# Optimization experiments

Measured on AMD Instinct MI355X. Metric: run time of the kernel, lower is better.

Reference implementation:

```python
import jax, jax.numpy as jnp
import numpy as np

COMMITMENT_COST = 0.25
NUM_EMBEDDINGS = 8192
EMBEDDING_DIM = 256


def setup_inputs() -> dict:
    key = jax.random.key(0)
    kx, ke = jax.random.split(key)
    x = jax.random.normal(kx, (16, 1024, EMBEDDING_DIM), dtype=jnp.float32)
    # nn.Embedding weight initialized uniform(-1/K, 1/K)
    embedding = jax.random.uniform(
        ke, (NUM_EMBEDDINGS, EMBEDDING_DIM), dtype=jnp.float32,
        minval=-1.0 / NUM_EMBEDDINGS, maxval=1.0 / NUM_EMBEDDINGS)
    return {"x": x, "embedding": embedding}


def reference(x, embedding):
    x_shape = x.shape
    D = embedding.shape[1]
    K = embedding.shape[0]
    flat_x = x.reshape(-1, D)                      # [N, D]
    N = flat_x.shape[0]

    distances = (jnp.sum(flat_x ** 2, axis=1, keepdims=True)
                 + jnp.sum(embedding ** 2, axis=1)
                 - 2.0 * jnp.matmul(flat_x, embedding.T))
    encoding_indices = jnp.argmin(distances, axis=1)  # [N]

    # one-hot @ embedding == gather
    quantized = embedding[encoding_indices].reshape(x_shape)

    sg = jax.lax.stop_gradient
    e_latent_loss = jnp.mean((sg(quantized) - x) ** 2)
    q_latent_loss = jnp.mean((quantized - sg(x)) ** 2)
    loss = q_latent_loss + COMMITMENT_COST * e_latent_loss

    # straight-through estimator
    quantized_st = x + sg(quantized - x)

    # perplexity from mean one-hot usage
    counts = jnp.zeros((K,), dtype=jnp.float32).at[encoding_indices].add(1.0)
    avg_probs = counts / N
    perplexity = jnp.exp(-jnp.sum(avg_probs * jnp.log(avg_probs + 1e-10)))

    return quantized_st.reshape(x_shape), loss, perplexity
```

## Files before the change

kernel.cpp:

```cpp
#include <hip/hip_runtime.h>


#define VQ_N 16384
#define VQ_D 256
#define VQ_K 8192

typedef __attribute__((ext_vector_type(4))) int i32x4;

#define SX 22.0f
#define SEF 1040384.0f
#define ENSCALE 11444224.0

__device__ inline int q8(float f, float scale) {
  return __float2int_rn(fminf(fmaxf(f * scale, -127.f), 127.f));
}

__device__ inline void gl_lds16(const void* g, void* l) {
  __builtin_amdgcn_global_load_lds(
      (const __attribute__((address_space(1))) unsigned int*)g,
      (__attribute__((address_space(3))) unsigned int*)l, 16, 0, 0);
}
__device__ inline void gl_lds4(const void* g, void* l) {
  __builtin_amdgcn_global_load_lds(
      (const __attribute__((address_space(1))) unsigned int*)g,
      (__attribute__((address_space(3))) unsigned int*)l, 4, 0, 0);
}

__global__ __launch_bounds__(256) void vq_pack(
    const float* __restrict__ E, signed char* __restrict__ Ebs,
    int* __restrict__ en_int, double* __restrict__ loss_sum,
    int* __restrict__ hist, unsigned int* __restrict__ ticket) {
  const int gid = blockIdx.x * 256 + threadIdx.x;
  if (gid < VQ_K) hist[gid] = 0;
  if (gid == 0) { *loss_sum = 0.0; *ticket = 0u; }
  const int code = gid >> 4;
  const int chunk = gid & 15;
  const float* src = E + (size_t)code * VQ_D + chunk * 16;
  double s = 0.0;
  unsigned int w[4];
#pragma unroll
  for (int v = 0; v < 4; ++v) {
    const float4 f = *(const float4*)(src + v * 4);
    s += (double)f.x * f.x + (double)f.y * f.y + (double)f.z * f.z +
         (double)f.w * f.w;
    const int q0 = q8(f.x, SEF), q1 = q8(f.y, SEF);
    const int q2 = q8(f.z, SEF), q3 = q8(f.w, SEF);
    w[v] = (unsigned)(q0 & 255) | ((unsigned)(q1 & 255) << 8) |
           ((unsigned)(q2 & 255) << 16) | ((unsigned)(q3 & 255) << 24);
  }
  const size_t off =
      ((size_t)(code >> 4) * 16 + chunk) * 256 + (size_t)(code & 15) * 16;
  *(uint4*)(Ebs + off) = make_uint4(w[0], w[1], w[2], w[3]);
#pragma unroll
  for (int m = 1; m <= 8; m <<= 1) s += __shfl_xor(s, m, 64);
  if (chunk == 0) en_int[code] = (int)__double2int_rn(s * ENSCALE);
}

__global__ __launch_bounds__(256, 2) void vq_score(
    const float* __restrict__ X, const signed char* __restrict__ Ebs,
    const int* __restrict__ en_int, unsigned long long* __restrict__ best64) {
  __shared__ __align__(16) signed char bbuf[2][16384];
  __shared__ __align__(16) int enl[1024];

  const int tid = threadIdx.x;
  const int wave = tid >> 6;
  const int lane = tid & 63;
  const int quad = lane >> 4;
  const int c15 = lane & 15;
  const int rowblk = blockIdx.x >> 3;
  const int q = blockIdx.x & 7;
  const int r0 = rowblk * 256;
  const int qcode = q * 1024;
  const signed char* ebase = Ebs + (size_t)qcode * 256;

  {
    const int* ens = en_int + qcode + wave * 64 + lane;
#pragma unroll
    for (int j = 0; j < 4; ++j)
      gl_lds4(ens + j * 256, enl + j * 256 + wave * 64);
    const signed char* bs = ebase + wave * 1024 + lane * 16;
#pragma unroll
    for (int j = 0; j < 4; ++j)
      gl_lds16(bs + j * 4096, &bbuf[0][j * 4096 + wave * 1024]);
  }

  i32x4 af[4][4];
#pragma unroll
  for (int t = 0; t < 4; ++t) {
    const float* xr =
        X + (size_t)(r0 + wave * 64 + t * 16 + c15) * VQ_D + quad * 16;
#pragma unroll
    for (int m = 0; m < 4; ++m) {
      const float* p = xr + m * 64;
      i32x4 pk;
#pragma unroll
      for (int v = 0; v < 4; ++v) {
        const float4 f = *(const float4*)(p + v * 4);
        pk[v] = (q8(f.x, SX) & 255) | ((q8(f.y, SX) & 255) << 8) |
                ((q8(f.z, SX) & 255) << 16) | ((q8(f.w, SX) & 255) << 24);
      }
      af[t][m] = pk;
    }
  }

  int best_s[4][4];
  int best_i[4][4];
#pragma unroll
  for (int t = 0; t < 4; ++t)
#pragma unroll
    for (int r = 0; r < 4; ++r) { best_s[t][r] = 0x7fffffff; best_i[t][r] = 0; }

#pragma unroll 1
  for (int c = 0; c < 16; ++c) {
    __syncthreads();
    if (c + 1 < 16) {
      const signed char* bs =
          ebase + (c + 1) * 16384 + wave * 1024 + lane * 16;
#pragma unroll
      for (int j = 0; j < 4; ++j)
        gl_lds16(bs + j * 4096, &bbuf[(c + 1) & 1][j * 4096 + wave * 1024]);
    }
    const signed char* cb = &bbuf[c & 1][0];
#pragma unroll
    for (int g = 0; g < 4; ++g) {
      i32x4 bfr[4];
#pragma unroll
      for (int m = 0; m < 4; ++m)
        bfr[m] = *(const i32x4*)(cb + g * 4096 + m * 1024 + lane * 16);
      const int en = enl[(c * 4 + g) * 16 + c15];
      i32x4 a0 = {0, 0, 0, 0}, a1 = {0, 0, 0, 0};
      i32x4 a2 = {0, 0, 0, 0}, a3 = {0, 0, 0, 0};
#pragma unroll
      for (int m = 0; m < 4; ++m) {
        a0 = __builtin_amdgcn_mfma_i32_16x16x64_i8(af[0][m], bfr[m], a0, 0, 0, 0);
        a1 = __builtin_amdgcn_mfma_i32_16x16x64_i8(af[1][m], bfr[m], a1, 0, 0, 0);
        a2 = __builtin_amdgcn_mfma_i32_16x16x64_i8(af[2][m], bfr[m], a2, 0, 0, 0);
        a3 = __builtin_amdgcn_mfma_i32_16x16x64_i8(af[3][m], bfr[m], a3, 0, 0, 0);
      }
      const int code = qcode + (c * 4 + g) * 16 + c15;
#pragma unroll
      for (int r = 0; r < 4; ++r) {
        int s;
        s = en - a0[r];
        if (s < best_s[0][r]) { best_s[0][r] = s; best_i[0][r] = code; }
        s = en - a1[r];
        if (s < best_s[1][r]) { best_s[1][r] = s; best_i[1][r] = code; }
        s = en - a2[r];
        if (s < best_s[2][r]) { best_s[2][r] = s; best_i[2][r] = code; }
        s = en - a3[r];
        if (s < best_s[3][r]) { best_s[3][r] = s; best_i[3][r] = code; }
      }
    }
  }

#pragma unroll
  for (int t = 0; t < 4; ++t)
#pragma unroll
    for (int r = 0; r < 4; ++r) {
      int s = best_s[t][r];
      int i = best_i[t][r];
#pragma unroll
      for (int m = 1; m <= 8; m <<= 1) {
        const int os = __shfl_xor(s, m, 64);
        const int oi = __shfl_xor(i, m, 64);
        if (os < s || (os == s && oi < i)) { s = os; i = oi; }
      }
      if (c15 == 0) {
        const int row = r0 + wave * 64 + t * 16 + quad * 4 + r;
        best64[(size_t)q * VQ_N + row] =
            ((unsigned long long)((unsigned)s ^ 0x80000000u) << 32) |
            (unsigned)i;
      }
    }
}

__global__ __launch_bounds__(256) void vq_gather_fin(
    const float* __restrict__ X, const float* __restrict__ E,
    const unsigned long long* __restrict__ best64, float* __restrict__ outq,
    double* __restrict__ loss_sum, int* __restrict__ hist,
    unsigned int* __restrict__ ticket, float* __restrict__ out) {
  __shared__ double wsum[4];
  __shared__ double part[256];
  __shared__ int sdone;
  const int wid = threadIdx.x >> 6;
  const int lane = threadIdx.x & 63;
  const int gw = blockIdx.x * 4 + wid;
  double acc = 0.0;
#pragma unroll 4
  for (int row = gw; row < VQ_N; row += 2048) {
    unsigned long long v =
        (lane < 8) ? best64[(size_t)lane * VQ_N + row] : ~0ULL;
#pragma unroll
    for (int m = 1; m <= 4; m <<= 1) {
      const unsigned long long ov = __shfl_xor(v, m, 64);
      if (ov < v) v = ov;
    }
    v = __shfl(v, 0, 64);
    const int k = (int)(v & 0xFFFFFFFFu);
    if (lane == 0)
      __hip_atomic_fetch_add(&hist[k], 1, __ATOMIC_RELAXED,
                             __HIP_MEMORY_SCOPE_AGENT);
    const float4 qv = *(const float4*)(E + (size_t)k * VQ_D + lane * 4);
    const float4 xv = *(const float4*)(X + (size_t)row * VQ_D + lane * 4);
    *(float4*)(outq + (size_t)row * VQ_D + lane * 4) = qv;
    const double dx = (double)qv.x - xv.x, dy = (double)qv.y - xv.y;
    const double dz = (double)qv.z - xv.z, dw = (double)qv.w - xv.w;
    acc += dx * dx + dy * dy + dz * dz + dw * dw;
  }
#pragma unroll
  for (int off = 32; off > 0; off >>= 1) acc += __shfl_down(acc, off, 64);
  if (lane == 0) wsum[wid] = acc;
  __syncthreads();
  if (threadIdx.x == 0) {
    atomicAdd(loss_sum, wsum[0] + wsum[1] + wsum[2] + wsum[3]);
    __threadfence();
    const unsigned int old = __hip_atomic_fetch_add(
        ticket, 1u, __ATOMIC_ACQ_REL, __HIP_MEMORY_SCOPE_AGENT);
    sdone = (old == 511u) ? 1 : 0;
  }
  __syncthreads();

  if (sdone) {
    const int tx = threadIdx.x;
    double s = 0.0;
    for (int k = tx; k < VQ_K; k += 256) {
      const int c = __hip_atomic_load(&hist[k], __ATOMIC_RELAXED,
                                      __HIP_MEMORY_SCOPE_AGENT);
      if (c > 0) {
        const double pr = (double)c * (1.0 / (double)VQ_N);
        s += pr * log(pr + 1e-10);
      }
    }
    part[tx] = s;
    __syncthreads();
    for (int off = 128; off > 0; off >>= 1) {
      if (tx < off) part[tx] += part[tx + off];
      __syncthreads();
    }
    if (tx == 0) {
      const double ls = __hip_atomic_load(loss_sum, __ATOMIC_RELAXED,
                                          __HIP_MEMORY_SCOPE_AGENT);
      out[(size_t)VQ_N * VQ_D] =
          (float)(1.25 * ls / ((double)VQ_N * (double)VQ_D));
      out[(size_t)VQ_N * VQ_D + 1] = (float)exp(-part[0]);
    }
  }
}

extern "C" void kernel_launch(void* const* d_in, const int* in_sizes, int n_in,
                              void* d_out, int out_size, void* d_ws,
                              size_t ws_size, hipStream_t stream) {
  const float* X = (const float*)d_in[0];
  const float* E = (const float*)d_in[1];
  float* out = (float*)d_out;

  char* ws = (char*)d_ws;
  signed char* Ebs = (signed char*)ws;
  int* en_int = (int*)(ws + 2097152);
  double* loss_sum = (double*)(ws + 2129920);
  int* hist = (int*)(ws + 2129984);
  unsigned int* ticket = (unsigned int*)(ws + 2162752);
  unsigned long long* best64 =
      (unsigned long long*)(ws + 2162816);

  vq_pack<<<512, 256, 0, stream>>>(E, Ebs, en_int, loss_sum, hist, ticket);
  vq_score<<<512, 256, 0, stream>>>(X, Ebs, en_int, best64);
  vq_gather_fin<<<512, 256, 0, stream>>>(X, E, best64, out, loss_sum, hist,
                                         ticket, out);
}
```

Baseline: 178.1 us.

## Fuse gather/finalize into score kernel and pack argmin index into score

Merges the gather and loss/perplexity stage into the scoring kernel. Blocks sharing a row block meet at a per-rowblock atomic spin barrier; each block then reduces and gathers 32 rows. The argmin loop is also simplified by packing the 64-group index into the low 6 bits of the score, so a single min replaces the compare-and-select of score and index. This removes one kernel launch and the separate pass over best64, but the spin barrier assumes all 8 blocks of a row block are co-resident, and shifting scores left by 6 risks int overflow.

```diff
diff --git a/kernel.cpp b/kernel.cpp
--- a/kernel.cpp
+++ b/kernel.cpp
@@ -29,10 +29,12 @@
 __global__ __launch_bounds__(256) void vq_pack(
     const float* __restrict__ E, signed char* __restrict__ Ebs,
     int* __restrict__ en_int, double* __restrict__ loss_sum,
-    int* __restrict__ hist, unsigned int* __restrict__ ticket) {
+    int* __restrict__ hist, unsigned int* __restrict__ tickrb,
+    unsigned int* __restrict__ ticket2) {
   const int gid = blockIdx.x * 256 + threadIdx.x;
   if (gid < VQ_K) hist[gid] = 0;
-  if (gid == 0) { *loss_sum = 0.0; *ticket = 0u; }
+  if (gid < 64) tickrb[gid] = 0u;
+  if (gid == 0) { *loss_sum = 0.0; *ticket2 = 0u; }
   const int code = gid >> 4;
   const int chunk = gid & 15;
   const float* src = E + (size_t)code * VQ_D + chunk * 16;
@@ -58,9 +60,16 @@
 
 __global__ __launch_bounds__(256, 2) void vq_score(
     const float* __restrict__ X, const signed char* __restrict__ Ebs,
-    const int* __restrict__ en_int, unsigned long long* __restrict__ best64) {
+    const int* __restrict__ en_int, const float* __restrict__ Ef,
+    float* __restrict__ outq, double* __restrict__ loss_sum,
+    int* __restrict__ hist, unsigned int* __restrict__ tickrb,
+    unsigned int* __restrict__ ticket2,
+    unsigned long long* __restrict__ bestp, float* __restrict__ out) {
   __shared__ __align__(16) signed char bbuf[2][16384];
   __shared__ __align__(16) int enl[1024];
+  __shared__ double wsum[4];
+  __shared__ double part[256];
+  __shared__ int sdone;
 
   const int tid = threadIdx.x;
   const int wave = tid >> 6;
@@ -103,12 +112,11 @@
     }
   }
 
-  int best_s[4][4];
-  int best_i[4][4];
+  int best_p[4][4];
 #pragma unroll
   for (int t = 0; t < 4; ++t)
 #pragma unroll
-    for (int r = 0; r < 4; ++r) { best_s[t][r] = 0x7fffffff; best_i[t][r] = 0; }
+    for (int r = 0; r < 4; ++r) best_p[t][r] = 0x7fffffff;
 
 #pragma unroll 1
   for (int c = 0; c < 16; ++c) {
@@ -127,7 +135,8 @@
 #pragma unroll
       for (int m = 0; m < 4; ++m)
         bfr[m] = *(const i32x4*)(cb + g * 4096 + m * 1024 + lane * 16);
-      const int en = enl[(c * 4 + g) * 16 + c15];
+      const int gidx = c * 4 + g;
+      const int enp = (enl[gidx * 16 + c15] << 6) + gidx;
       i32x4 a0 = {0, 0, 0, 0}, a1 = {0, 0, 0, 0};
       i32x4 a2 = {0, 0, 0, 0}, a3 = {0, 0, 0, 0};
 #pragma unroll
@@ -137,18 +146,12 @@
         a2 = __builtin_amdgcn_mfma_i32_16x16x64_i8(af[2][m], bfr[m], a2, 0, 0, 0);
         a3 = __builtin_amdgcn_mfma_i32_16x16x64_i8(af[3][m], bfr[m], a3, 0, 0, 0);
       }
-      const int code = qcode + (c * 4 + g) * 16 + c15;
 #pragma unroll
       for (int r = 0; r < 4; ++r) {
-        int s;
-        s = en - a0[r];
-        if (s < best_s[0][r]) { best_s[0][r] = s; best_i[0][r] = code; }
-        s = en - a1[r];
-        if (s < best_s[1][r]) { best_s[1][r] = s; best_i[1][r] = code; }
-        s = en - a2[r];
-        if (s < best_s[2][r]) { best_s[2][r] = s; best_i[2][r] = code; }
-        s = en - a3[r];
-        if (s < best_s[3][r]) { best_s[3][r] = s; best_i[3][r] = code; }
+        best_p[0][r] = min(best_p[0][r], enp - (a0[r] << 6));
+        best_p[1][r] = min(best_p[1][r], enp - (a1[r] << 6));
+        best_p[2][r] = min(best_p[2][r], enp - (a2[r] << 6));
+        best_p[3][r] = min(best_p[3][r], enp - (a3[r] << 6));
       }
     }
   }
@@ -157,39 +160,41 @@
   for (int t = 0; t < 4; ++t)
 #pragma unroll
     for (int r = 0; r < 4; ++r) {
-      int s = best_s[t][r];
-      int i = best_i[t][r];
+      const int p = best_p[t][r];
+      const int s = p >> 6;
+      const int code = qcode + (p & 63) * 16 + c15;
+      unsigned long long v =
+          ((unsigned long long)((unsigned)s ^ 0x80000000u) << 32) |
+          (unsigned)code;
 #pragma unroll
       for (int m = 1; m <= 8; m <<= 1) {
-        const int os = __shfl_xor(s, m, 64);
-        const int oi = __shfl_xor(i, m, 64);
-        if (os < s || (os == s && oi < i)) { s = os; i = oi; }
+        const unsigned long long ov = __shfl_xor(v, m, 64);
+        if (ov < v) v = ov;
       }
       if (c15 == 0) {
         const int row = r0 + wave * 64 + t * 16 + quad * 4 + r;
-        best64[(size_t)q * VQ_N + row] =
-            ((unsigned long long)((unsigned)s ^ 0x80000000u) << 32) |
-            (unsigned)i;
-      }
-    }
-}
-
-__global__ __launch_bounds__(256) void vq_gather_fin(
-    const float* __restrict__ X, const float* __restrict__ E,
-    const unsigned long long* __restrict__ best64, float* __restrict__ outq,
-    double* __restrict__ loss_sum, int* __restrict__ hist,
-    unsigned int* __restrict__ ticket, float* __restrict__ out) {
-  __shared__ double wsum[4];
-  __shared__ double part[256];
-  __shared__ int sdone;
-  const int wid = threadIdx.x >> 6;
-  const int lane = threadIdx.x & 63;
-  const int gw = blockIdx.x * 4 + wid;
-  double acc = 0.0;
-#pragma unroll 4
-  for (int row = gw; row < VQ_N; row += 2048) {
+        bestp[(size_t)row * 8 + q] = v;
+      }
+    }
+
+  __threadfence();
+  __syncthreads();
+  if (tid == 0) {
+    __hip_atomic_fetch_add(&tickrb[rowblk], 1u, __ATOMIC_ACQ_REL,
+                           __HIP_MEMORY_SCOPE_AGENT);
+    while (__hip_atomic_load(&tickrb[rowblk], __ATOMIC_ACQUIRE,
+                             __HIP_MEMORY_SCOPE_AGENT) < 8u)
+      __builtin_amdgcn_s_sleep(2);
+  }
+  __syncthreads();
+
+  const int myr0 = r0 + q * 32;
+  double lacc = 0.0;
+#pragma unroll
+  for (int j = 0; j < 8; ++j) {
+    const int row = myr0 + wave * 8 + j;
     unsigned long long v =
-        (lane < 8) ? best64[(size_t)lane * VQ_N + row] : ~0ULL;
+        (lane < 8) ? bestp[(size_t)row * 8 + lane] : ~0ULL;
 #pragma unroll
     for (int m = 1; m <= 4; m <<= 1) {
       const unsigned long long ov = __shfl_xor(v, m, 64);
@@ -200,30 +205,29 @@
     if (lane == 0)
       __hip_atomic_fetch_add(&hist[k], 1, __ATOMIC_RELAXED,
                              __HIP_MEMORY_SCOPE_AGENT);
-    const float4 qv = *(const float4*)(E + (size_t)k * VQ_D + lane * 4);
+    const float4 qv = *(const float4*)(Ef + (size_t)k * VQ_D + lane * 4);
     const float4 xv = *(const float4*)(X + (size_t)row * VQ_D + lane * 4);
     *(float4*)(outq + (size_t)row * VQ_D + lane * 4) = qv;
     const double dx = (double)qv.x - xv.x, dy = (double)qv.y - xv.y;
     const double dz = (double)qv.z - xv.z, dw = (double)qv.w - xv.w;
-    acc += dx * dx + dy * dy + dz * dz + dw * dw;
-  }
-#pragma unroll
-  for (int off = 32; off > 0; off >>= 1) acc += __shfl_down(acc, off, 64);
-  if (lane == 0) wsum[wid] = acc;
-  __syncthreads();
-  if (threadIdx.x == 0) {
+    lacc += dx * dx + dy * dy + dz * dz + dw * dw;
+  }
+#pragma unroll
+  for (int off = 32; off > 0; off >>= 1) lacc += __shfl_down(lacc, off, 64);
+  if (lane == 0) wsum[wave] = lacc;
+  __syncthreads();
+  if (tid == 0) {
     atomicAdd(loss_sum, wsum[0] + wsum[1] + wsum[2] + wsum[3]);
     __threadfence();
     const unsigned int old = __hip_atomic_fetch_add(
-        ticket, 1u, __ATOMIC_ACQ_REL, __HIP_MEMORY_SCOPE_AGENT);
+        ticket2, 1u, __ATOMIC_ACQ_REL, __HIP_MEMORY_SCOPE_AGENT);
     sdone = (old == 511u) ? 1 : 0;
   }
   __syncthreads();
 
   if (sdone) {
-    const int tx = threadIdx.x;
     double s = 0.0;
-    for (int k = tx; k < VQ_K; k += 256) {
+    for (int k = tid; k < VQ_K; k += 256) {
       const int c = __hip_atomic_load(&hist[k], __ATOMIC_RELAXED,
                                       __HIP_MEMORY_SCOPE_AGENT);
       if (c > 0) {
@@ -231,13 +235,13 @@
         s += pr * log(pr + 1e-10);
       }
     }
-    part[tx] = s;
+    part[tid] = s;
     __syncthreads();
     for (int off = 128; off > 0; off >>= 1) {
-      if (tx < off) part[tx] += part[tx + off];
+      if (tid < off) part[tid] += part[tid + off];
       __syncthreads();
     }
-    if (tx == 0) {
+    if (tid == 0) {
       const double ls = __hip_atomic_load(loss_sum, __ATOMIC_RELAXED,
                                           __HIP_MEMORY_SCOPE_AGENT);
       out[(size_t)VQ_N * VQ_D] =
@@ -259,12 +263,13 @@
   int* en_int = (int*)(ws + 2097152);
   double* loss_sum = (double*)(ws + 2129920);
   int* hist = (int*)(ws + 2129984);
-  unsigned int* ticket = (unsigned int*)(ws + 2162752);
-  unsigned long long* best64 =
-      (unsigned long long*)(ws + 2162816);
-
-  vq_pack<<<512, 256, 0, stream>>>(E, Ebs, en_int, loss_sum, hist, ticket);
-  vq_score<<<512, 256, 0, stream>>>(X, Ebs, en_int, best64);
-  vq_gather_fin<<<512, 256, 0, stream>>>(X, E, best64, out, loss_sum, hist,
-                                         ticket, out);
-}
+  unsigned int* ticket2 = (unsigned int*)(ws + 2162752);
+  unsigned int* tickrb = (unsigned int*)(ws + 2162816);
+  unsigned long long* bestp =
+      (unsigned long long*)(ws + 2163072);
+
+  vq_pack<<<512, 256, 0, stream>>>(E, Ebs, en_int, loss_sum, hist, tickrb,
+                                   ticket2);
+  vq_score<<<512, 256, 0, stream>>>(X, Ebs, en_int, E, out, loss_sum, hist,
+                                    tickrb, ticket2, bestp, out);
+}
```

After: 246.7 us. 1.39x slower.

## Pack argmin index into score word, use 512-thread blocks and atomicMin reduction

Applied to the files above, without the earlier changes.

The score kernel now runs 512-thread blocks with 8 waves, each wave holding 2 row tiles instead of 4, and stages twice as much codebook per LDS buffer. The argmin tracking packs the tile index into the low 6 bits of the shifted score, so a single integer min replaces the compare-and-select pair. Per-row results from the 8 codebook slices are merged with a 64-bit atomicMin into one array, so the gather kernel reads one word per row instead of reducing 8. The cost is atomic traffic in the score kernel and shifted scores that could overflow if values are large, plus a different LDS footprint that may change occupancy.

```diff
diff --git a/kernel.cpp b/kernel.cpp
--- a/kernel.cpp
+++ b/kernel.cpp
@@ -29,9 +29,11 @@
 __global__ __launch_bounds__(256) void vq_pack(
     const float* __restrict__ E, signed char* __restrict__ Ebs,
     int* __restrict__ en_int, double* __restrict__ loss_sum,
-    int* __restrict__ hist, unsigned int* __restrict__ ticket) {
+    int* __restrict__ hist, unsigned long long* __restrict__ bestfin,
+    unsigned int* __restrict__ ticket) {
   const int gid = blockIdx.x * 256 + threadIdx.x;
   if (gid < VQ_K) hist[gid] = 0;
+  if (gid < VQ_N) bestfin[gid] = ~0ULL;
   if (gid == 0) { *loss_sum = 0.0; *ticket = 0u; }
   const int code = gid >> 4;
   const int chunk = gid & 15;
@@ -56,10 +58,11 @@
   if (chunk == 0) en_int[code] = (int)__double2int_rn(s * ENSCALE);
 }
 
-__global__ __launch_bounds__(256, 2) void vq_score(
+__global__ __launch_bounds__(512, 2) void vq_score(
     const float* __restrict__ X, const signed char* __restrict__ Ebs,
-    const int* __restrict__ en_int, unsigned long long* __restrict__ best64) {
-  __shared__ __align__(16) signed char bbuf[2][16384];
+    const int* __restrict__ en_int,
+    unsigned long long* __restrict__ bestfin) {
+  __shared__ __align__(16) signed char bbuf[2][32768];
   __shared__ __align__(16) int enl[1024];
 
   const int tid = threadIdx.x;
@@ -74,21 +77,22 @@
   const signed char* ebase = Ebs + (size_t)qcode * 256;
 
   {
-    const int* ens = en_int + qcode + wave * 64 + lane;
+    const int* ens = en_int + qcode;
+#pragma unroll
+    for (int j = 0; j < 2; ++j)
+      gl_lds4(ens + j * 512 + wave * 64 + lane,
+              enl + j * 512 + wave * 64 + lane);
 #pragma unroll
     for (int j = 0; j < 4; ++j)
-      gl_lds4(ens + j * 256, enl + j * 256 + wave * 64);
-    const signed char* bs = ebase + wave * 1024 + lane * 16;
-#pragma unroll
-    for (int j = 0; j < 4; ++j)
-      gl_lds16(bs + j * 4096, &bbuf[0][j * 4096 + wave * 1024]);
-  }
-
-  i32x4 af[4][4];
-#pragma unroll
-  for (int t = 0; t < 4; ++t) {
+      gl_lds16(ebase + j * 8192 + wave * 1024 + lane * 16,
+               &bbuf[0][j * 8192 + wave * 1024 + lane * 16]);
+  }
+
+  i32x4 af[2][4];
+#pragma unroll
+  for (int t = 0; t < 2; ++t) {
     const float* xr =
-        X + (size_t)(r0 + wave * 64 + t * 16 + c15) * VQ_D + quad * 16;
+        X + (size_t)(r0 + wave * 32 + t * 16 + c15) * VQ_D + quad * 16;
 #pragma unroll
     for (int m = 0; m < 4; ++m) {
       const float* p = xr + m * 64;
@@ -103,80 +107,70 @@
     }
   }
 
-  int best_s[4][4];
-  int best_i[4][4];
-#pragma unroll
-  for (int t = 0; t < 4; ++t)
-#pragma unroll
-    for (int r = 0; r < 4; ++r) { best_s[t][r] = 0x7fffffff; best_i[t][r] = 0; }
+  int best_p[2][4];
+#pragma unroll
+  for (int t = 0; t < 2; ++t)
+#pragma unroll
+    for (int r = 0; r < 4; ++r) best_p[t][r] = 0x7fffffff;
 
 #pragma unroll 1
-  for (int c = 0; c < 16; ++c) {
+  for (int c = 0; c < 8; ++c) {
     __syncthreads();
-    if (c + 1 < 16) {
-      const signed char* bs =
-          ebase + (c + 1) * 16384 + wave * 1024 + lane * 16;
+    if (c + 1 < 8) {
+      const signed char* bs = ebase + (c + 1) * 32768;
 #pragma unroll
       for (int j = 0; j < 4; ++j)
-        gl_lds16(bs + j * 4096, &bbuf[(c + 1) & 1][j * 4096 + wave * 1024]);
+        gl_lds16(bs + j * 8192 + wave * 1024 + lane * 16,
+                 &bbuf[(c + 1) & 1][j * 8192 + wave * 1024 + lane * 16]);
     }
     const signed char* cb = &bbuf[c & 1][0];
 #pragma unroll
-    for (int g = 0; g < 4; ++g) {
+    for (int g = 0; g < 8; ++g) {
       i32x4 bfr[4];
 #pragma unroll
       for (int m = 0; m < 4; ++m)
         bfr[m] = *(const i32x4*)(cb + g * 4096 + m * 1024 + lane * 16);
-      const int en = enl[(c * 4 + g) * 16 + c15];
+      const int gidx = c * 8 + g;
+      const int enp = (enl[gidx * 16 + c15] << 6) + gidx;
       i32x4 a0 = {0, 0, 0, 0}, a1 = {0, 0, 0, 0};
-      i32x4 a2 = {0, 0, 0, 0}, a3 = {0, 0, 0, 0};
 #pragma unroll
       for (int m = 0; m < 4; ++m) {
         a0 = __builtin_amdgcn_mfma_i32_16x16x64_i8(af[0][m], bfr[m], a0, 0, 0, 0);
         a1 = __builtin_amdgcn_mfma_i32_16x16x64_i8(af[1][m], bfr[m], a1, 0, 0, 0);
-        a2 = __builtin_amdgcn_mfma_i32_16x16x64_i8(af[2][m], bfr[m], a2, 0, 0, 0);
-        a3 = __builtin_amdgcn_mfma_i32_16x16x64_i8(af[3][m], bfr[m], a3, 0, 0, 0);
-      }
-      const int code = qcode + (c * 4 + g) * 16 + c15;
+      }
 #pragma unroll
       for (int r = 0; r < 4; ++r) {
-        int s;
-        s = en - a0[r];
-        if (s < best_s[0][r]) { best_s[0][r] = s; best_i[0][r] = code; }
-        s = en - a1[r];
-        if (s < best_s[1][r]) { best_s[1][r] = s; best_i[1][r] = code; }
-        s = en - a2[r];
-        if (s < best_s[2][r]) { best_s[2][r] = s; best_i[2][r] = code; }
-        s = en - a3[r];
-        if (s < best_s[3][r]) { best_s[3][r] = s; best_i[3][r] = code; }
-      }
-    }
-  }
-
-#pragma unroll
-  for (int t = 0; t < 4; ++t)
+        best_p[0][r] = min(best_p[0][r], enp - (a0[r] << 6));
+        best_p[1][r] = min(best_p[1][r], enp - (a1[r] << 6));
+      }
+    }
+  }
+
+#pragma unroll
+  for (int t = 0; t < 2; ++t)
 #pragma unroll
     for (int r = 0; r < 4; ++r) {
-      int s = best_s[t][r];
-      int i = best_i[t][r];
+      const int p = best_p[t][r];
+      const int s = p >> 6;
+      const int code = qcode + (p & 63) * 16 + c15;
+      unsigned long long v =
+          ((unsigned long long)((unsigned)s ^ 0x80000000u) << 32) |
+          (unsigned)code;
 #pragma unroll
       for (int m = 1; m <= 8; m <<= 1) {
-        const int os = __shfl_xor(s, m, 64);
-        const int oi = __shfl_xor(i, m, 64);
-        if (os < s || (os == s && oi < i)) { s = os; i = oi; }
+        const unsigned long long ov = __shfl_xor(v, m, 64);
+        if (ov < v) v = ov;
       }
       if (c15 == 0) {
-        const int row = r0 + wave * 64 + t * 16 + quad * 4 + r;
-        best64[(size_t)q * VQ_N + row] =
-            ((unsigned long long)((unsigned)s ^ 0x80000000u) << 32) |
-            (unsigned)i;
+        const int row = r0 + wave * 32 + t * 16 + quad * 4 + r;
+        atomicMin(&bestfin[row], v);
       }
     }
 }
 
 __global__ __launch_bounds__(256) void vq_gather_fin(
     const float* __restrict__ X, const float* __restrict__ E,
-    const unsigned long long* __restrict__ best64, float* __restrict__ outq,
+    const unsigned long long* __restrict__ bestfin, float* __restrict__ outq,
     double* __restrict__ loss_sum, int* __restrict__ hist,
     unsigned int* __restrict__ ticket, float* __restrict__ out) {
   __shared__ double wsum[4];
@@ -185,21 +179,26 @@
   const int wid = threadIdx.x >> 6;
   const int lane = threadIdx.x & 63;
   const int gw = blockIdx.x * 4 + wid;
+  const int row0 = gw * 8;
+
+  const unsigned long long v = (lane < 8) ? bestfin[row0 + lane] : 0ULL;
+  int ks[8];
+#pragma unroll
+  for (int j = 0; j < 8; ++j)
+    ks[j] = (int)(__shfl(v, j, 64) & 0xFFFFFFFFu);
+
+  if (lane == 0) {
+#pragma unroll
+    for (int j = 0; j < 8; ++j)
+      __hip_atomic_fetch_add(&hist[ks[j]], 1, __ATOMIC_RELAXED,
+                             __HIP_MEMORY_SCOPE_AGENT);
+  }
+
   double acc = 0.0;
-#pragma unroll 4
-  for (int row = gw; row < VQ_N; row += 2048) {
-    unsigned long long v =
-        (lane < 8) ? best64[(size_t)lane * VQ_N + row] : ~0ULL;
-#pragma unroll
-    for (int m = 1; m <= 4; m <<= 1) {
-      const unsigned long long ov = __shfl_xor(v, m, 64);
-      if (ov < v) v = ov;
-    }
-    v = __shfl(v, 0, 64);
-    const int k = (int)(v & 0xFFFFFFFFu);
-    if (lane == 0)
-      __hip_atomic_fetch_add(&hist[k], 1, __ATOMIC_RELAXED,
-                             __HIP_MEMORY_SCOPE_AGENT);
+#pragma unroll
+  for (int j = 0; j < 8; ++j) {
+    const int row = row0 + j;
+    const int k = ks[j];
     const float4 qv = *(const float4*)(E + (size_t)k * VQ_D + lane * 4);
     const float4 xv = *(const float4*)(X + (size_t)row * VQ_D + lane * 4);
     *(float4*)(outq + (size_t)row * VQ_D + lane * 4) = qv;
@@ -260,11 +259,12 @@
   double* loss_sum = (double*)(ws + 2129920);
   int* hist = (int*)(ws + 2129984);
   unsigned int* ticket = (unsigned int*)(ws + 2162752);
-  unsigned long long* best64 =
+  unsigned long long* bestfin =
       (unsigned long long*)(ws + 2162816);
 
-  vq_pack<<<512, 256, 0, stream>>>(E, Ebs, en_int, loss_sum, hist, ticket);
-  vq_score<<<512, 256, 0, stream>>>(X, Ebs, en_int, best64);
-  vq_gather_fin<<<512, 256, 0, stream>>>(X, E, best64, out, loss_sum, hist,
+  vq_pack<<<512, 256, 0, stream>>>(E, Ebs, en_int, loss_sum, hist, bestfin,
+                                   ticket);
+  vq_score<<<512, 512, 0, stream>>>(X, Ebs, en_int, bestfin);
+  vq_gather_fin<<<512, 256, 0, stream>>>(X, E, bestfin, out, loss_sum, hist,
                                          ticket, out);
 }
```

Result: faster. 166.3 us (-6.6%).
